# Optimization experiments

Hardware: AMD Instinct MI355X
Metric: run time of the kernel (lower is better)

Reference implementation:

```python
import jax, jax.numpy as jnp
import numpy as np

B, T, D = 2, 2048, 2048
NH, NKV, HD = 16, 4, 128
EPS = 1e-6
ROPE_THETA = 10000.0


def rms_norm(x, w):
    # per-head RMSNorm over the last (head_dim) axis
    var = jnp.mean(jnp.square(x), axis=-1, keepdims=True)
    return x * jax.lax.rsqrt(var + EPS) * w


def rope_sin_cos(seq_len, dim, dtype):
    inv_freq = 1.0 / (ROPE_THETA ** (jnp.arange(0, dim, 2, dtype=jnp.float32) / dim))
    t = jnp.arange(seq_len, dtype=jnp.float32)
    ang = jnp.outer(t, inv_freq)                      # [T, HD/2]
    ang = jnp.concatenate([ang, ang], axis=-1)         # [T, HD]
    return jnp.sin(ang).astype(dtype), jnp.cos(ang).astype(dtype)


def rotate_half(x):
    x1, x2 = jnp.split(x, 2, axis=-1)
    return jnp.concatenate([-x2, x1], axis=-1)


def apply_rope(x, sin, cos):
    # x: [B, T, H, HD]; sin/cos: [T, HD]
    s = sin[None, :, None, :]
    c = cos[None, :, None, :]
    return x * c + rotate_half(x) * s


def setup_inputs() -> dict:
    key = jax.random.key(0)
    ks = jax.random.split(key, 5)
    scale = 1.0 / np.sqrt(D)
    return {
        "x": jax.random.normal(ks[0], (B, T, D), jnp.float32),
        "wq": jax.random.normal(ks[1], (D, D), jnp.float32) * scale,
        "wk": jax.random.normal(ks[2], (NKV * HD, D), jnp.float32) * scale,
        "wv": jax.random.normal(ks[3], (NKV * HD, D), jnp.float32) * scale,
        "wo": jax.random.normal(ks[4], (D, D), jnp.float32) * scale,
        "q_norm_w": jnp.ones((HD,), jnp.float32),
        "k_norm_w": jnp.ones((HD,), jnp.float32),
    }


def reference(x, wq, wk, wv, wo, q_norm_w, k_norm_w):
    b, t, _ = x.shape
    q = (x @ wq.T).reshape(b, t, NH, HD)    # [B,T,NH,HD]
    k = (x @ wk.T).reshape(b, t, NKV, HD)   # [B,T,NKV,HD]
    v = (x @ wv.T).reshape(b, t, NKV, HD)

    # per-head QK RMS norm
    q = rms_norm(q, q_norm_w)
    k = rms_norm(k, k_norm_w)

    # RoPE
    sin, cos = rope_sin_cos(t, HD, x.dtype)
    q = apply_rope(q, sin, cos)
    k = apply_rope(k, sin, cos)

    # GQA: expand kv heads to match query heads
    rep = NH // NKV
    k = jnp.repeat(k, rep, axis=2)          # [B,T,NH,HD]
    v = jnp.repeat(v, rep, axis=2)

    # causal SDPA
    scale = 1.0 / np.sqrt(HD)
    scores = jnp.einsum('bqhd,bkhd->bhqk', q, k) * scale
    causal = jnp.tril(jnp.ones((t, t), bool))
    scores = jnp.where(causal[None, None], scores, jnp.finfo(scores.dtype).min)
    probs = jax.nn.softmax(scores, axis=-1)
    att = jnp.einsum('bhqk,bkhd->bqhd', probs, v).reshape(b, t, NH * HD)
    return att @ wo.T
```

## Files before the change

kernel.cpp:

```cpp
#include <hip/hip_runtime.h>
#include <hip/hip_bf16.h>

#define B_ 2
#define T_ 2048
#define D_ 2048
#define NH_ 16
#define NKV_ 4
#define HD_ 128

using bf16 = __bf16;
using bf16x8 = __attribute__((ext_vector_type(8))) __bf16;
using bf16x4 = __attribute__((ext_vector_type(4))) __bf16;
using f32x4 = __attribute__((ext_vector_type(4))) float;

__device__ __forceinline__ void gld_lds16(bf16* lds, const bf16* g) {
  __builtin_amdgcn_global_load_lds(
      (const __attribute__((address_space(1))) void*)g,
      (__attribute__((address_space(3))) void*)lds, 16, 0, 0);
}

__global__ __launch_bounds__(256) void cvt_all(const float* __restrict__ x,
                                               const float* __restrict__ wq,
                                               const float* __restrict__ wk,
                                               const float* __restrict__ wv,
                                               const float* __restrict__ wo,
                                               bf16* __restrict__ xb,
                                               bf16* __restrict__ wqkvb,
                                               bf16* __restrict__ wob) {
  const int bid = blockIdx.x;
  const float* src;
  bf16* dst;
  int base;
  if (bid < 8192)       { src = x;  dst = xb;              base = bid; }
  else if (bid < 12288) { src = wq; dst = wqkvb;           base = bid - 8192; }
  else if (bid < 13312) { src = wk; dst = wqkvb + 4194304; base = bid - 12288; }
  else if (bid < 14336) { src = wv; dst = wqkvb + 5242880; base = bid - 13312; }
  else                  { src = wo; dst = wob;             base = bid - 14336; }
  const int i = base * 256 + threadIdx.x;
  float4 v = ((const float4*)src)[i];
  bf16x4 o;
  o[0] = (bf16)v.x; o[1] = (bf16)v.y; o[2] = (bf16)v.z; o[3] = (bf16)v.w;
  ((bf16x4*)dst)[i] = o;
}

template<typename OutT>
__global__ __launch_bounds__(256) void gemm_bt(const bf16* __restrict__ A,
                                               const bf16* __restrict__ Bt,
                                               OutT* __restrict__ C,
                                               int M, int N, int K) {
  __shared__ bf16 As[3][128 * 32];
  __shared__ bf16 Bs[3][128 * 32];
  const int tid = threadIdx.x;
  const int wid = tid >> 6;
  const int lane = tid & 63;
  const int g = lane >> 4, r = lane & 15;
  const int wm = wid >> 1, wn = wid & 1;
  const int gx = gridDim.x;
  const int nwg = gx * gridDim.y;
  const int flat = blockIdx.y * gx + blockIdx.x;
  const int swz = (flat & 7) * (nwg >> 3) + (flat >> 3);
  const long bm = (long)(swz / gx) * 128, bn = (long)(swz % gx) * 128;
  f32x4 acc[4][4] = {};
  const int NT = K >> 5;

  auto stage = [&](int buf, int k0) {
    for (int c = 0; c < 2; ++c) {
      int ch = wid * 2 + c;
      int row = ch * 16 + (lane >> 2);
      int col = (lane & 3) * 8;
      gld_lds16(&As[buf][ch * 512], A + (bm + row) * K + k0 + col);
      gld_lds16(&Bs[buf][ch * 512], Bt + (bn + row) * K + k0 + col);
    }
  };

  stage(0, 0);
  stage(1, 32);
  for (int t = 0; t < NT; ++t) {
    if (t + 1 < NT)
      asm volatile("s_waitcnt vmcnt(4)" ::: "memory");
    else
      asm volatile("s_waitcnt vmcnt(0)" ::: "memory");
    __builtin_amdgcn_s_barrier();
    if (t + 2 < NT) stage((t + 2) % 3, (t + 2) * 32);
    const bf16* as = As[t % 3];
    const bf16* bs = Bs[t % 3];
    bf16x8 af[4], bfr[4];
    for (int m = 0; m < 4; ++m)
      af[m] = *(const bf16x8*)(as + (wm * 64 + m * 16 + r) * 32 + g * 8);
    for (int n = 0; n < 4; ++n)
      bfr[n] = *(const bf16x8*)(bs + (wn * 64 + n * 16 + r) * 32 + g * 8);
    for (int m = 0; m < 4; ++m)
      for (int n = 0; n < 4; ++n)
        acc[m][n] = __builtin_amdgcn_mfma_f32_16x16x32_bf16(af[m], bfr[n], acc[m][n], 0, 0, 0);
  }

  for (int m = 0; m < 4; ++m)
    for (int n = 0; n < 4; ++n)
      for (int e = 0; e < 4; ++e) {
        long row = bm + wm * 64 + m * 16 + g * 4 + e;
        long col = bn + wn * 64 + n * 16 + r;
        C[row * N + col] = (OutT)acc[m][n][e];
      }
}

__global__ __launch_bounds__(256) void norm_rope_qk(const bf16* __restrict__ qkv,
                                                    const float* __restrict__ qw,
                                                    const float* __restrict__ kw,
                                                    bf16* __restrict__ Qb,
                                                    bf16* __restrict__ Kb) {
  const int lane = threadIdx.x & 63;
  const int rloc = threadIdx.x >> 6;
  const int bid = blockIdx.x;
  const int IS_K = bid >= 16384;
  const int NHH = IS_K ? NKV_ : NH_;
  const int COFF = IS_K ? 2048 : 0;
  const float* w = IS_K ? kw : qw;
  const long rid = (long)(IS_K ? bid - 16384 : bid) * 4 + rloc;
  const int h = (int)(rid % NHH);
  const long bt = rid / NHH;
  const int t = (int)(bt % T_);
  const bf16* src = qkv + bt * 3072 + COFF + h * HD_;
  float v0 = (float)src[lane];
  float v1 = (float)src[lane + 64];
  float ss = v0 * v0 + v1 * v1;
  for (int o = 1; o < 64; o <<= 1) ss += __shfl_xor(ss, o, 64);
  float inv = rsqrtf(ss * (1.f / HD_) + 1e-6f);
  float n0 = v0 * inv * w[lane];
  float n1 = v1 * inv * w[lane + 64];
  float ang = (float)t * exp2f((float)lane * (-13.287712379549449f / 64.f));
  float sv, cv;
  __sincosf(ang, &sv, &cv);
  float o0 = n0 * cv - n1 * sv;
  float o1 = n1 * cv + n0 * sv;
  bf16* dst;
  if (IS_K) {
    long b = bt / T_;
    dst = Kb + ((b * NKV_ + h) * (long)T_ + t) * HD_;
  } else {
    dst = Qb + (bt * NH_ + h) * HD_;
  }
  dst[lane] = (bf16)o0;
  dst[lane + 64] = (bf16)o1;
}

__global__ __launch_bounds__(256) void vpack(const bf16* __restrict__ qkv,
                                             bf16* __restrict__ Vt) {
  __shared__ float tile[64][65];
  const int tt = blockIdx.x;
  const int dd = blockIdx.y & 1;
  const int bkv = blockIdx.y >> 1;
  const long b = bkv >> 2;
  const int kv = bkv & 3;
  const int t0 = tt * 64, d0 = dd * 64;
  for (int i = 0; i < 2; ++i) {
    int row = i * 32 + (threadIdx.x >> 3);
    int c8 = (threadIdx.x & 7) * 8;
    bf16x8 v = *(const bf16x8*)&qkv[(b * T_ + t0 + row) * 3072 + 2560 + kv * HD_ + d0 + c8];
    for (int j = 0; j < 8; ++j) tile[row][c8 + j] = (float)v[j];
  }
  __syncthreads();
  for (int i = 0; i < 2; ++i) {
    int drow = i * 32 + (threadIdx.x >> 3);
    int tc8 = (threadIdx.x & 7) * 8;
    bf16x8 o;
    for (int j = 0; j < 8; ++j) o[j] = (bf16)tile[tc8 + j][drow];
    *(bf16x8*)&Vt[((b * NKV_ + kv) * (long)HD_ + d0 + drow) * T_ + t0 + tc8] = o;
  }
}

__global__ __launch_bounds__(512) void flash_attn(const bf16* __restrict__ Q,
                                                  const bf16* __restrict__ K,
                                                  const bf16* __restrict__ V,
                                                  bf16* __restrict__ O) {
  __shared__ bf16 Ks[2][64 * 128];
  __shared__ bf16 Vs[2][128 * 64];
  __shared__ bf16 Ps[8][16 * 64];
  const int h = blockIdx.y, b = blockIdx.z;
  const int qt = b ? blockIdx.x : (gridDim.x - 1) - blockIdx.x;
  const int kv = h >> 2;
  const int tid = threadIdx.x, wid = tid >> 6, lane = tid & 63;
  const int g = lane >> 4, r = lane & 15;
  const int q0 = qt * 128;
  const int qbase = q0 + wid * 16;
  const int q = qbase + r;

  bf16x8 aq[4];
  const bf16* qp = Q + ((long)(b * T_ + q)) * (NH_ * HD_) + h * HD_;
  for (int kk = 0; kk < 4; ++kk) aq[kk] = *(const bf16x8*)(qp + kk * 32 + g * 8);

  f32x4 oacc[8] = {};
  float m_run = -1e30f, l_run = 0.f;

  const bf16* Kbase = K + ((long)(b * NKV_ + kv)) * T_ * HD_;
  const bf16* Vbase = V + ((long)(b * NKV_ + kv)) * (long)HD_ * T_;
  const int nkt = 2 * qt + 2;

  auto stageKV = [&](int buf, int k0) {
    for (int c = 0; c < 2; ++c) {
      int ch = wid * 2 + c;
      {
        int row = ch * 4 + (lane >> 4);
        int srccol = ((lane & 15) ^ (row & 7)) * 8;
        gld_lds16(&Ks[buf][ch * 512], Kbase + (long)(k0 + row) * HD_ + srccol);
      }
      {
        int row = ch * 8 + (lane >> 3);
        int srccol = ((lane & 7) ^ (row & 7)) * 8;
        gld_lds16(&Vs[buf][ch * 512], Vbase + (long)row * T_ + k0 + srccol);
      }
    }
  };

  stageKV(0, 0);
  for (int kt = 0; kt < nkt; ++kt) {
    const int k0 = kt * 64;
    const int cur = kt & 1;
    if (kt + 1 < nkt) {
      stageKV(cur ^ 1, k0 + 64);
      asm volatile("s_waitcnt vmcnt(4)" ::: "memory");
    } else {
      asm volatile("s_waitcnt vmcnt(0)" ::: "memory");
    }
    __builtin_amdgcn_s_barrier();

    f32x4 s[4] = {};
    __builtin_amdgcn_s_setprio(1);
    for (int n = 0; n < 4; ++n)
      for (int kk = 0; kk < 4; ++kk) {
        int row = n * 16 + r;
        bf16x8 bk = *(const bf16x8*)(&Ks[cur][row * 128 + (((kk * 4 + g) ^ (row & 7)) * 8)]);
        s[n] = __builtin_amdgcn_mfma_f32_16x16x32_bf16(bk, aq[kk], s[n], 0, 0, 0);
      }
    __builtin_amdgcn_s_setprio(0);

    const float scale = 0.088388347648318447f;
    const bool domask = (k0 + 63 > qbase);

    for (int hh = 0; hh < 2; ++hh) {
      float mx = -1e30f;
      if (domask) {
        for (int n = 2 * hh; n < 2 * hh + 2; ++n) {
          const int km = k0 + n * 16 + g * 4;
          for (int e = 0; e < 4; ++e) {
            float v = s[n][e] * scale;
            if (km + e > q) v = -1e30f;
            s[n][e] = v;
            mx = fmaxf(mx, v);
          }
        }
      } else {
        for (int n = 2 * hh; n < 2 * hh + 2; ++n)
          for (int e = 0; e < 4; ++e) {
            float v = s[n][e] * scale;
            s[n][e] = v;
            mx = fmaxf(mx, v);
          }
      }
      mx = fmaxf(mx, __shfl_xor(mx, 16, 64));
      mx = fmaxf(mx, __shfl_xor(mx, 32, 64));
      float mnew = fmaxf(m_run, mx);
      float alpha = __expf(m_run - mnew);
      float ls = 0.f;
      for (int n = 2 * hh; n < 2 * hh + 2; ++n) {
        bf16x4 pb;
        for (int e = 0; e < 4; ++e) {
          float p = __expf(s[n][e] - mnew);
          ls += p;
          pb[e] = (bf16)p;
        }
        int c = n * 2 + (g >> 1);
        *(bf16x4*)(&Ps[wid][r * 64 + ((c ^ (r & 7)) * 8) + (g & 1) * 4]) = pb;
      }
      ls += __shfl_xor(ls, 16, 64);
      ls += __shfl_xor(ls, 32, 64);
      m_run = mnew;
      l_run = l_run * alpha + ls;

      float al[4];
      for (int e = 0; e < 4; ++e)
        al[e] = __shfl(alpha, (lane & 48) | (g * 4 + e), 64);
      for (int dt = 0; dt < 8; ++dt)
        for (int e = 0; e < 4; ++e) oacc[dt][e] *= al[e];

      asm volatile("s_waitcnt lgkmcnt(0)" ::: "memory");

      __builtin_amdgcn_s_setprio(1);
      bf16x8 ap = *(const bf16x8*)(&Ps[wid][r * 64 + (((hh * 4 + g) ^ (r & 7)) * 8)]);
      for (int dt = 0; dt < 8; ++dt) {
        int row = dt * 16 + r;
        bf16x8 bv = *(const bf16x8*)(&Vs[cur][row * 64 + (((hh * 4 + g) ^ (row & 7)) * 8)]);
        oacc[dt] = __builtin_amdgcn_mfma_f32_16x16x32_bf16(ap, bv, oacc[dt], 0, 0, 0);
      }
      __builtin_amdgcn_s_setprio(0);
    }
    __builtin_amdgcn_s_barrier();
  }

  float li[4];
  for (int e = 0; e < 4; ++e) {
    float lv = __shfl(l_run, (lane & 48) | (g * 4 + e), 64);
    li[e] = 1.f / lv;
  }
  for (int e = 0; e < 4; ++e) {
    const int grow = q0 + wid * 16 + g * 4 + e;
    bf16* dst = O + ((long)(b * T_ + grow)) * (NH_ * HD_) + h * HD_;
    for (int dt = 0; dt < 8; ++dt)
      dst[dt * 16 + r] = (bf16)(oacc[dt][e] * li[e]);
  }
}

extern "C" void kernel_launch(void* const* d_in, const int* in_sizes, int n_in,
                              void* d_out, int out_size, void* d_ws, size_t ws_size,
                              hipStream_t stream) {
  const float* x  = (const float*)d_in[0];
  const float* wq = (const float*)d_in[1];
  const float* wk = (const float*)d_in[2];
  const float* wv = (const float*)d_in[3];
  const float* wo = (const float*)d_in[4];
  const float* qw = (const float*)d_in[5];
  const float* kw = (const float*)d_in[6];
  float* out = (float*)d_out;

  char* p = (char*)d_ws;
  bf16* xb    = (bf16*)(p);
  bf16* wqkvb = (bf16*)(p + 16777216);
  bf16* wob   = (bf16*)(p + 29360128);
  bf16* QKVr  = (bf16*)(p + 37748736);
  bf16* Qb    = (bf16*)(p + 62914560);
  bf16* Kb    = (bf16*)(p + 79691776);
  bf16* Vt    = (bf16*)(p + 83886080);
  bf16* attb  = (bf16*)(p + 88080384);

  cvt_all<<<18432, 256, 0, stream>>>(x, wq, wk, wv, wo, xb, wqkvb, wob);

  gemm_bt<bf16><<<dim3(24, 32), 256, 0, stream>>>(xb, wqkvb, QKVr, 4096, 3072, 2048);

  norm_rope_qk<<<20480, 256, 0, stream>>>(QKVr, qw, kw, Qb, Kb);
  vpack<<<dim3(32, 16), 256, 0, stream>>>(QKVr, Vt);

  flash_attn<<<dim3(16, 16, 2), 512, 0, stream>>>(Qb, Kb, Vt, attb);

  gemm_bt<float><<<dim3(16, 32), 256, 0, stream>>>(attb, wob, out, 4096, 2048, 2048);
}
```

Measured before the change: 224.9 us.

## Have each flash-attention wave process two 16-row query tiles to reuse K/V fragments

```diff
diff --git a/kernel.cpp b/kernel.cpp
--- a/kernel.cpp
+++ b/kernel.cpp
@@ -168,7 +168,7 @@
   }
 }
 
-__global__ __launch_bounds__(512) void flash_attn(const bf16* __restrict__ Q,
+__global__ __launch_bounds__(256) void flash_attn(const bf16* __restrict__ Q,
                                                   const bf16* __restrict__ K,
                                                   const bf16* __restrict__ V,
                                                   bf16* __restrict__ O) {
@@ -181,23 +181,29 @@
   const int tid = threadIdx.x, wid = tid >> 6, lane = tid & 63;
   const int g = lane >> 4, r = lane & 15;
   const int q0 = qt * 128;
-  const int qbase = q0 + wid * 16;
-  const int q = qbase + r;
-
-  bf16x8 aq[4];
-  const bf16* qp = Q + ((long)(b * T_ + q)) * (NH_ * HD_) + h * HD_;
-  for (int kk = 0; kk < 4; ++kk) aq[kk] = *(const bf16x8*)(qp + kk * 32 + g * 8);
-
-  f32x4 oacc[8] = {};
-  float m_run = -1e30f, l_run = 0.f;
+  const int qbaseA = q0 + wid * 32;
+  const int qbaseB = qbaseA + 16;
+  const int qA = qbaseA + r;
+  const int qB = qbaseB + r;
+
+  bf16x8 aqA[4], aqB[4];
+  const bf16* qpA = Q + ((long)(b * T_ + qA)) * (NH_ * HD_) + h * HD_;
+  const bf16* qpB = Q + ((long)(b * T_ + qB)) * (NH_ * HD_) + h * HD_;
+  for (int kk = 0; kk < 4; ++kk) {
+    aqA[kk] = *(const bf16x8*)(qpA + kk * 32 + g * 8);
+    aqB[kk] = *(const bf16x8*)(qpB + kk * 32 + g * 8);
+  }
+
+  f32x4 oaccA[8] = {}, oaccB[8] = {};
+  float mA = -1e30f, lA = 0.f, mB = -1e30f, lB = 0.f;
 
   const bf16* Kbase = K + ((long)(b * NKV_ + kv)) * T_ * HD_;
   const bf16* Vbase = V + ((long)(b * NKV_ + kv)) * (long)HD_ * T_;
   const int nkt = 2 * qt + 2;
 
   auto stageKV = [&](int buf, int k0) {
-    for (int c = 0; c < 2; ++c) {
-      int ch = wid * 2 + c;
+    for (int c = 0; c < 4; ++c) {
+      int ch = wid * 4 + c;
       {
         int row = ch * 4 + (lane >> 4);
         int srccol = ((lane & 15) ^ (row & 7)) * 8;
@@ -210,6 +216,8 @@
       }
     }
   };
+
+  const float scale = 0.088388347648318447f;
 
   stageKV(0, 0);
   for (int kt = 0; kt < nkt; ++kt) {
@@ -217,39 +225,40 @@
     const int cur = kt & 1;
     if (kt + 1 < nkt) {
       stageKV(cur ^ 1, k0 + 64);
-      asm volatile("s_waitcnt vmcnt(4)" ::: "memory");
+      asm volatile("s_waitcnt vmcnt(8)" ::: "memory");
     } else {
       asm volatile("s_waitcnt vmcnt(0)" ::: "memory");
     }
     __builtin_amdgcn_s_barrier();
 
-    f32x4 s[4] = {};
+    f32x4 sA[4] = {}, sB[4] = {};
     __builtin_amdgcn_s_setprio(1);
     for (int n = 0; n < 4; ++n)
       for (int kk = 0; kk < 4; ++kk) {
         int row = n * 16 + r;
         bf16x8 bk = *(const bf16x8*)(&Ks[cur][row * 128 + (((kk * 4 + g) ^ (row & 7)) * 8)]);
-        s[n] = __builtin_amdgcn_mfma_f32_16x16x32_bf16(bk, aq[kk], s[n], 0, 0, 0);
+        sA[n] = __builtin_amdgcn_mfma_f32_16x16x32_bf16(bk, aqA[kk], sA[n], 0, 0, 0);
+        sB[n] = __builtin_amdgcn_mfma_f32_16x16x32_bf16(bk, aqB[kk], sB[n], 0, 0, 0);
       }
     __builtin_amdgcn_s_setprio(0);
 
-    const float scale = 0.088388347648318447f;
-    const bool domask = (k0 + 63 > qbase);
-
-    for (int hh = 0; hh < 2; ++hh) {
+    auto softmax_half = [&](f32x4 (&s)[4], float& m_run, float& l_run,
+                            const int qq, const int qbase, bf16* ps,
+                            f32x4 (&oacc)[8]) {
+      const bool domask = (k0 + 63 > qbase);
       float mx = -1e30f;
       if (domask) {
-        for (int n = 2 * hh; n < 2 * hh + 2; ++n) {
+        for (int n = 0; n < 4; ++n) {
           const int km = k0 + n * 16 + g * 4;
           for (int e = 0; e < 4; ++e) {
             float v = s[n][e] * scale;
-            if (km + e > q) v = -1e30f;
+            if (km + e > qq) v = -1e30f;
             s[n][e] = v;
             mx = fmaxf(mx, v);
           }
         }
       } else {
-        for (int n = 2 * hh; n < 2 * hh + 2; ++n)
+        for (int n = 0; n < 4; ++n)
           for (int e = 0; e < 4; ++e) {
             float v = s[n][e] * scale;
             s[n][e] = v;
@@ -261,7 +270,7 @@
       float mnew = fmaxf(m_run, mx);
       float alpha = __expf(m_run - mnew);
       float ls = 0.f;
-      for (int n = 2 * hh; n < 2 * hh + 2; ++n) {
+      for (int n = 0; n < 4; ++n) {
         bf16x4 pb;
         for (int e = 0; e < 4; ++e) {
           float p = __expf(s[n][e] - mnew);
@@ -269,43 +278,54 @@
           pb[e] = (bf16)p;
         }
         int c = n * 2 + (g >> 1);
-        *(bf16x4*)(&Ps[wid][r * 64 + ((c ^ (r & 7)) * 8) + (g & 1) * 4]) = pb;
+        *(bf16x4*)(&ps[r * 64 + ((c ^ (r & 7)) * 8) + (g & 1) * 4]) = pb;
       }
       ls += __shfl_xor(ls, 16, 64);
       ls += __shfl_xor(ls, 32, 64);
       m_run = mnew;
       l_run = l_run * alpha + ls;
-
       float al[4];
       for (int e = 0; e < 4; ++e)
         al[e] = __shfl(alpha, (lane & 48) | (g * 4 + e), 64);
       for (int dt = 0; dt < 8; ++dt)
         for (int e = 0; e < 4; ++e) oacc[dt][e] *= al[e];
-
-      asm volatile("s_waitcnt lgkmcnt(0)" ::: "memory");
-
-      __builtin_amdgcn_s_setprio(1);
-      bf16x8 ap = *(const bf16x8*)(&Ps[wid][r * 64 + (((hh * 4 + g) ^ (r & 7)) * 8)]);
+    };
+    softmax_half(sA, mA, lA, qA, qbaseA, &Ps[wid * 2][0], oaccA);
+    softmax_half(sB, mB, lB, qB, qbaseB, &Ps[wid * 2 + 1][0], oaccB);
+
+    asm volatile("s_waitcnt lgkmcnt(0)" ::: "memory");
+
+    __builtin_amdgcn_s_setprio(1);
+    for (int kk = 0; kk < 2; ++kk) {
+      bf16x8 apA = *(const bf16x8*)(&Ps[wid * 2][r * 64 + (((kk * 4 + g) ^ (r & 7)) * 8)]);
+      bf16x8 apB = *(const bf16x8*)(&Ps[wid * 2 + 1][r * 64 + (((kk * 4 + g) ^ (r & 7)) * 8)]);
       for (int dt = 0; dt < 8; ++dt) {
         int row = dt * 16 + r;
-        bf16x8 bv = *(const bf16x8*)(&Vs[cur][row * 64 + (((hh * 4 + g) ^ (row & 7)) * 8)]);
-        oacc[dt] = __builtin_amdgcn_mfma_f32_16x16x32_bf16(ap, bv, oacc[dt], 0, 0, 0);
-      }
-      __builtin_amdgcn_s_setprio(0);
+        bf16x8 bv = *(const bf16x8*)(&Vs[cur][row * 64 + (((kk * 4 + g) ^ (row & 7)) * 8)]);
+        oaccA[dt] = __builtin_amdgcn_mfma_f32_16x16x32_bf16(apA, bv, oaccA[dt], 0, 0, 0);
+        oaccB[dt] = __builtin_amdgcn_mfma_f32_16x16x32_bf16(apB, bv, oaccB[dt], 0, 0, 0);
+      }
     }
+    __builtin_amdgcn_s_setprio(0);
     __builtin_amdgcn_s_barrier();
   }
 
-  float li[4];
+  float liA[4], liB[4];
   for (int e = 0; e < 4; ++e) {
-    float lv = __shfl(l_run, (lane & 48) | (g * 4 + e), 64);
-    li[e] = 1.f / lv;
+    float lvA = __shfl(lA, (lane & 48) | (g * 4 + e), 64);
+    float lvB = __shfl(lB, (lane & 48) | (g * 4 + e), 64);
+    liA[e] = 1.f / lvA;
+    liB[e] = 1.f / lvB;
   }
   for (int e = 0; e < 4; ++e) {
-    const int grow = q0 + wid * 16 + g * 4 + e;
-    bf16* dst = O + ((long)(b * T_ + grow)) * (NH_ * HD_) + h * HD_;
+    const int growA = qbaseA + g * 4 + e;
+    bf16* dstA = O + ((long)(b * T_ + growA)) * (NH_ * HD_) + h * HD_;
     for (int dt = 0; dt < 8; ++dt)
-      dst[dt * 16 + r] = (bf16)(oacc[dt][e] * li[e]);
+      dstA[dt * 16 + r] = (bf16)(oaccA[dt][e] * liA[e]);
+    const int growB = qbaseB + g * 4 + e;
+    bf16* dstB = O + ((long)(b * T_ + growB)) * (NH_ * HD_) + h * HD_;
+    for (int dt = 0; dt < 8; ++dt)
+      dstB[dt * 16 + r] = (bf16)(oaccB[dt][e] * liB[e]);
   }
 }
 
@@ -338,7 +358,7 @@
   norm_rope_qk<<<20480, 256, 0, stream>>>(QKVr, qw, kw, Qb, Kb);
   vpack<<<dim3(32, 16), 256, 0, stream>>>(QKVr, Vt);
 
-  flash_attn<<<dim3(16, 16, 2), 512, 0, stream>>>(Qb, Kb, Vt, attb);
+  flash_attn<<<dim3(16, 16, 2), 256, 0, stream>>>(Qb, Kb, Vt, attb);
 
   gemm_bt<float><<<dim3(16, 32), 256, 0, stream>>>(attb, wob, out, 4096, 2048, 2048);
 }
```

New measurement: 275.2 us. +22.4%, slower.
